# Performance work log

Measured on AMD Instinct MI355X. Metric: run time of the kernel, lower is better.

The kernel has to match this reference:

```python
import jax, jax.numpy as jnp
import numpy as np

B, S, H, DH = 4, 2048, 16, 64
D = H * DH          # 1024
EXP = 2
FF_IN = EXP * D * 2  # 4096 (SwiGLU doubles)
FF_HID = EXP * D     # 2048
SCALE_BASE = 512
LN_EPS = 1e-5


def setup_inputs() -> dict:
    key = jax.random.key(0)
    ks = jax.random.split(key, 8)
    inp = {
        "q": jax.random.normal(ks[0], (B, S, D), jnp.float32),
        "k": jax.random.normal(ks[1], (B, S, D), jnp.float32),
        "v": jax.random.normal(ks[2], (B, S, D), jnp.float32),
        "Wqkv": jax.random.normal(ks[3], (D, 3 * D), jnp.float32) * (1.0 / np.sqrt(D)),
        "bqkv": jnp.zeros((3 * D,), jnp.float32),
        "q_scale": jnp.ones((DH,), jnp.float32),
        "k_scale": jnp.ones((DH,), jnp.float32),
        "ln_g": jnp.ones((D,), jnp.float32),
        "ln_b": jnp.zeros((D,), jnp.float32),
        "W1": jax.random.normal(ks[4], (D, FF_IN), jnp.float32) * (1.0 / np.sqrt(D)),
        "b1": jnp.zeros((FF_IN,), jnp.float32),
        "W2": jax.random.normal(ks[5], (FF_HID, D), jnp.float32) * (1.0 / np.sqrt(FF_HID)),
        "b2": jnp.zeros((D,), jnp.float32),
    }
    return inp


def rotate_half(x):
    x1, x2 = jnp.split(x, 2, axis=-1)
    return jnp.concatenate((-x2, x1), axis=-1)


def apply_rope(pos, t, scale):
    # pos: [S, DH], scale: [S, DH] (broadcast over [B, H, S, DH])
    return t * jnp.cos(pos) * scale + rotate_half(t) * jnp.sin(pos) * scale


def rotary_tables(seq_len):
    inv_freq = 1.0 / (10000.0 ** (jnp.arange(0, DH, 2, dtype=jnp.float32) / DH))
    t = jnp.arange(seq_len, dtype=jnp.float32)
    freqs = t[:, None] * inv_freq[None, :]            # [S, DH/2]
    freqs = jnp.concatenate((freqs, freqs), axis=-1)  # [S, DH]
    power = (t - seq_len // 2) / SCALE_BASE           # [S]
    base = (jnp.arange(0, DH, 2, dtype=jnp.float32) + 0.4 * DH) / (1.4 * DH)  # [DH/2]
    scale = base[None, :] ** power[:, None]           # [S, DH/2]
    scale = jnp.concatenate((scale, scale), axis=-1)  # [S, DH]
    return freqs, scale


def l2norm(x, eps=1e-12):
    n = jnp.sqrt(jnp.sum(x * x, axis=-1, keepdims=True))
    return x / jnp.maximum(n, eps)


def reference(q, k, v, Wqkv, bqkv, q_scale, k_scale, ln_g, ln_b, W1, b1, W2, b2):
    del k, v  # module projects qkv from q; k,v args are unused (faithful to source)
    n, seq_len, _ = q.shape
    qkv = q @ Wqkv + bqkv                              # [B, S, 3D]
    qkv = qkv.reshape(n, seq_len, H, 3 * DH).transpose(0, 2, 1, 3)  # [B, H, S, 3DH]
    q_, k_, v_ = jnp.split(qkv, 3, axis=-1)
    q_ = l2norm(q_) * q_scale
    k_ = l2norm(k_) * k_scale
    pos, xscale = rotary_tables(seq_len)
    q_ = apply_rope(pos, q_, xscale)
    k_ = apply_rope(pos, k_, 1.0 / xscale)
    # scaled dot product attention (non-causal)
    scores = jnp.einsum("bhid,bhjd->bhij", q_, k_) / np.sqrt(DH)
    attn = jax.nn.softmax(scores, axis=-1)
    out = jnp.einsum("bhij,bhjd->bhid", attn, v_)      # [B, H, S, DH]
    out = out.transpose(0, 2, 1, 3).reshape(n, seq_len, D)
    # LayerNorm
    mu = jnp.mean(out, axis=-1, keepdims=True)
    var = jnp.mean((out - mu) ** 2, axis=-1, keepdims=True)
    out = (out - mu) / jnp.sqrt(var + LN_EPS) * ln_g + ln_b
    # SwiGLU FFN (dropout = identity in eval)
    h = out @ W1 + b1                                  # [B, S, FF_IN]
    x_, gate = jnp.split(h, 2, axis=-1)
    ff = (jax.nn.silu(gate) * x_) @ W2 + b2            # [B, S, D]
    return out + ff
```

## Files before the change

### kernel.cpp

```cpp
#include <hip/hip_runtime.h>
#include <math.h>


typedef __bf16 bf16;
typedef bf16 bf16x8 __attribute__((ext_vector_type(8)));
typedef bf16 bf16x4 __attribute__((ext_vector_type(4)));
typedef float f32x4 __attribute__((ext_vector_type(4)));

#define MFMA(a, b, c) __builtin_amdgcn_mfma_f32_16x16x32_bf16(a, b, c, 0, 0, 0)

__device__ __forceinline__ void async16(const void* g, void* l) {
    __builtin_amdgcn_global_load_lds(
        (const __attribute__((address_space(1))) void*)g,
        (__attribute__((address_space(3))) void*)l,
        16, 0, 0);
}

__global__ __launch_bounds__(256) void fill_sentinel(float* __restrict__ o)
{
    size_t i = ((size_t)blockIdx.x * 256 + threadIdx.x) * 4;
    *(float4*)&o[i] = make_float4(0.25f, 0.25f, 0.25f, 0.25f);
}

__global__ __launch_bounds__(256) void transpose_f32_bf16(
    const float* __restrict__ in, bf16* __restrict__ out, int K, int N)
{
    __shared__ bf16 T[64][70];
    const int tN = N >> 6;
    const int tk = blockIdx.x / tN, tn = blockIdx.x % tN;
    const int k0 = tk << 6, n0 = tn << 6;
    const int t = threadIdx.x;
    const int r = t >> 2, c0 = (t & 3) << 4;
    const float* src = &in[(size_t)(k0 + r) * N + n0 + c0];
    for (int j = 0; j < 4; ++j) {
        float4 f = *(const float4*)(src + 4 * j);
        T[r][c0 + 4 * j + 0] = (bf16)f.x;
        T[r][c0 + 4 * j + 1] = (bf16)f.y;
        T[r][c0 + 4 * j + 2] = (bf16)f.z;
        T[r][c0 + 4 * j + 3] = (bf16)f.w;
    }
    __syncthreads();
    bf16x8 o0, o1;
    for (int i = 0; i < 8; ++i) o0[i] = T[c0 + i][r];
    for (int i = 0; i < 8; ++i) o1[i] = T[c0 + 8 + i][r];
    *(bf16x8*)&out[(size_t)(n0 + r) * K + k0 + c0]     = o0;
    *(bf16x8*)&out[(size_t)(n0 + r) * K + k0 + c0 + 8] = o1;
}

__global__ __launch_bounds__(256) void transpose_v(
    const bf16* __restrict__ in, bf16* __restrict__ out)
{
    __shared__ bf16 T[64][72];
    const int bh = blockIdx.x >> 5;
    const int s0 = (blockIdx.x & 31) << 6;
    const bf16* ip = in + ((size_t)bh << 17) + (size_t)s0 * 64;
    bf16* op = out + ((size_t)bh << 17) + s0;
    const int t = threadIdx.x;
    const int r = t >> 2, c0 = (t & 3) << 4;
    *(bf16x8*)&T[r][c0]     = *(const bf16x8*)&ip[r * 64 + c0];
    *(bf16x8*)&T[r][c0 + 8] = *(const bf16x8*)&ip[r * 64 + c0 + 8];
    __syncthreads();
    bf16x8 o0, o1;
    for (int i = 0; i < 8; ++i) o0[i] = T[c0 + i][r];
    for (int i = 0; i < 8; ++i) o1[i] = T[c0 + 8 + i][r];
    *(bf16x8*)&op[(size_t)r * 2048 + c0]     = o0;
    *(bf16x8*)&op[(size_t)r * 2048 + c0 + 8] = o1;
}

template <int EPI, bool AF32>
__global__ __launch_bounds__(256) void gemm_bt(
    const void* __restrict__ Avp, const bf16* __restrict__ BT,
    const float* __restrict__ bias, int M, int N, int K, int lda,
    bf16* __restrict__ C0, bf16* __restrict__ C1, bf16* __restrict__ C2,
    float* __restrict__ Cf, const bf16* __restrict__ resid)
{
    __shared__ bf16 As[128 * 64];
    __shared__ bf16 Bs[128 * 64];
    const int tid = threadIdx.x;
    const int lane = tid & 63, wave = tid >> 6;
    const int quad = lane >> 4, l16 = lane & 15;
    const int wm = wave >> 1, wn = wave & 1;
    const int nb = N >> 7;
    const int bm = blockIdx.x / nb, bn = blockIdx.x % nb;
    const int m0 = bm << 7, n0 = bn << 7;
    const float* Af = (const float*)Avp;
    const bf16*  Ab = (const bf16*)Avp;
    char* aB = (char*)&As[0];
    char* bB = (char*)&Bs[0];
    const int rsw = l16 & 7;

    f32x4 acc[4][4] = {};

    for (int kt = 0; kt < K; kt += 64) {
        for (int i = 0; i < 4; ++i) {
            int l = (i << 8) + tid;
            int r = l >> 3;
            int cbs = ((l & 7) ^ (r & 7)) << 3;
            int cu = (i << 8) + (wave << 6);
            if (!AF32)
                async16(&Ab[(size_t)(m0 + r) * lda + kt + cbs], aB + (size_t)cu * 16);
            async16(&BT[(size_t)(n0 + r) * K + kt + cbs], bB + (size_t)cu * 16);
        }
        if (AF32) {
            for (int i = 0; i < 4; ++i) {
                int l = (i << 8) + tid;
                int r = l >> 3;
                int cbs = ((l & 7) ^ (r & 7)) << 3;
                const float* s = &Af[(size_t)(m0 + r) * lda + kt + cbs];
                float4 f0 = *(const float4*)s;
                float4 f1 = *(const float4*)(s + 4);
                bf16x8 tv;
                tv[0] = (bf16)f0.x; tv[1] = (bf16)f0.y;
                tv[2] = (bf16)f0.z; tv[3] = (bf16)f0.w;
                tv[4] = (bf16)f1.x; tv[5] = (bf16)f1.y;
                tv[6] = (bf16)f1.z; tv[7] = (bf16)f1.w;
                *(bf16x8*)&As[l << 3] = tv;
            }
        }
        __syncthreads();
        for (int kd = 0; kd < 2; ++kd) {
            bf16x8 af[4], bfr[4];
            for (int mi = 0; mi < 4; ++mi) {
                int row = (wm << 6) + (mi << 4) + l16;
                af[mi] = *(const bf16x8*)&As[(row << 6) + ((((kd << 2) + quad) ^ rsw) << 3)];
            }
            for (int ni = 0; ni < 4; ++ni) {
                int row = (wn << 6) + (ni << 4) + l16;
                bfr[ni] = *(const bf16x8*)&Bs[(row << 6) + ((((kd << 2) + quad) ^ rsw) << 3)];
            }
            for (int mi = 0; mi < 4; ++mi)
                for (int ni = 0; ni < 4; ++ni)
                    acc[mi][ni] = MFMA(af[mi], bfr[ni], acc[mi][ni]);
        }
        __syncthreads();
    }

    for (int mi = 0; mi < 4; ++mi) {
        for (int ni = 0; ni < 4; ++ni) {
            for (int r = 0; r < 4; ++r) {
                int row = m0 + (wm << 6) + (mi << 4) + (quad << 2) + r;
                int col = n0 + (wn << 6) + (ni << 4) + l16;
                float v = acc[mi][ni][r] + bias[col];
                if (EPI == 0) {
                    int b = row >> 11, s = row & 2047;
                    int h = col / 192, w = col % 192;
                    int tq = w >> 6, d = w & 63;
                    bf16* dst = (tq == 0) ? C0 : (tq == 1) ? C1 : C2;
                    dst[((((size_t)b * 16 + h) * 2048 + s) << 6) + d] = (bf16)v;
                } else if (EPI == 1) {
                    C0[(size_t)row * N + col] = (bf16)v;
                } else {
                    float rv = (float)resid[(size_t)row * N + col];
                    Cf[(size_t)row * N + col] = v + rv;
                }
            }
        }
    }
}

__global__ __launch_bounds__(256) void norm_rope(
    bf16* __restrict__ qb, bf16* __restrict__ kb,
    const float* __restrict__ qs, const float* __restrict__ ks)
{
    const int wave = threadIdx.x >> 6, lane = threadIdx.x & 63;
    const int rid = blockIdx.x * 4 + wave;
    const bool is_k = rid >= 131072;
    const int idx = is_k ? rid - 131072 : rid;
    const int s = idx & 2047;
    bf16* ptr = (is_k ? kb : qb) + ((size_t)idx << 6);
    const int d = lane;

    float v = (float)ptr[d];
    float ss = v * v;
    for (int o = 1; o < 64; o <<= 1) ss += __shfl_xor(ss, o);
    float t = v * rsqrtf(fmaxf(ss, 1e-24f));
    t *= (is_k ? ks : qs)[d];

    float partner = __shfl_xor(t, 32);
    float rh = (d < 32) ? -partner : partner;

    const float fi = (float)(d & 31);
    float inv_freq = __builtin_amdgcn_exp2f(fi * -0.4152410118609203f);
    float pos = (float)s * inv_freq;
    float rev = pos * 0.15915494309189535f;
    rev = rev - floorf(rev);
    float sn = __builtin_amdgcn_sinf(rev);
    float cs = __builtin_amdgcn_cosf(rev);
    float base = (2.0f * fi + 25.6f) * (1.0f / 89.6f);
    float power = ((float)s - 1024.0f) * (1.0f / 512.0f);
    if (is_k) power = -power;
    float xsc = __builtin_amdgcn_exp2f(power * __builtin_amdgcn_logf(base));
    ptr[d] = (bf16)((t * cs + rh * sn) * xsc);
}

__global__ __launch_bounds__(256) void attn(
    const bf16* __restrict__ Q, const bf16* __restrict__ Kb,
    const bf16* __restrict__ VT, bf16* __restrict__ O)
{
    __shared__ bf16 Ks[64 * 64];
    __shared__ bf16 Vt[64 * 64];
    __shared__ bf16 Ps[4][2][16][72];
    const int tid = threadIdx.x;
    const int lane = tid & 63, wave = tid >> 6;
    const int quad = lane >> 4, l16 = lane & 15;
    const int rsw = l16 & 7;
    const int bh = blockIdx.x >> 4;
    const int q0 = (blockIdx.x & 15) << 7;
    const int s_base = q0 + (wave << 5);
    const bf16* Qp = Q + ((size_t)bh << 17);
    const bf16* Kp = Kb + ((size_t)bh << 17);
    const bf16* Vp = VT + ((size_t)bh << 17);

    bf16x8 qf[2][2];
    for (int sub = 0; sub < 2; ++sub) {
        const bf16* qrow = Qp + (size_t)(s_base + (sub << 4) + l16) * 64;
        qf[sub][0] = *(const bf16x8*)&qrow[(quad << 3)];
        qf[sub][1] = *(const bf16x8*)&qrow[32 + (quad << 3)];
        for (int j = 0; j < 8; ++j) {
            qf[sub][0][j] = (bf16)((float)qf[sub][0][j] * 0.1803368801f);
            qf[sub][1][j] = (bf16)((float)qf[sub][1][j] * 0.1803368801f);
        }
    }
    bf16x8 ones = {};
    if (l16 == 0) for (int j = 0; j < 8; ++j) ones[j] = (bf16)1.0f;

    f32x4 oacc[2][4] = {};
    f32x4 lacc[2] = {};
    char* kB = (char*)&Ks[0];
    char* vB = (char*)&Vt[0];

    for (int kt = 0; kt < 2048; kt += 64) {
        __syncthreads();
        for (int i = 0; i < 2; ++i) {
            int l = (i << 8) + tid;
            int r = l >> 3;
            int cbs = ((l & 7) ^ (r & 7)) << 3;
            int cu = (i << 8) + (wave << 6);
            async16(&Kp[(size_t)(kt + r) * 64 + cbs], kB + (size_t)cu * 16);
            async16(&Vp[(size_t)r * 2048 + kt + cbs], vB + (size_t)cu * 16);
        }
        __syncthreads();

        f32x4 sc[2][4];
        for (int nt = 0; nt < 4; ++nt) {
            int row = (nt << 4) + l16;
            bf16x8 kf0 = *(const bf16x8*)&Ks[(row << 6) + ((quad ^ rsw) << 3)];
            bf16x8 kf1 = *(const bf16x8*)&Ks[(row << 6) + (((quad + 4) ^ rsw) << 3)];
            for (int sub = 0; sub < 2; ++sub) {
                f32x4 z = {};
                z = MFMA(qf[sub][0], kf0, z);
                z = MFMA(qf[sub][1], kf1, z);
                sc[sub][nt] = z;
            }
        }
        const int prow = quad << 2;
        for (int sub = 0; sub < 2; ++sub)
            for (int r = 0; r < 4; ++r)
                for (int nt = 0; nt < 4; ++nt)
                    Ps[wave][sub][prow + r][(nt << 4) + l16] =
                        (bf16)__builtin_amdgcn_exp2f(sc[sub][nt][r]);
        __builtin_amdgcn_wave_barrier();
        bf16x8 pf0[2], pf1[2];
        for (int sub = 0; sub < 2; ++sub) {
            pf0[sub] = *(const bf16x8*)&Ps[wave][sub][l16][(quad << 3)];
            pf1[sub] = *(const bf16x8*)&Ps[wave][sub][l16][32 + (quad << 3)];
        }
        for (int ntd = 0; ntd < 4; ++ntd) {
            int row = (ntd << 4) + l16;
            bf16x8 vf0 = *(const bf16x8*)&Vt[(row << 6) + ((quad ^ rsw) << 3)];
            bf16x8 vf1 = *(const bf16x8*)&Vt[(row << 6) + (((quad + 4) ^ rsw) << 3)];
            for (int sub = 0; sub < 2; ++sub) {
                oacc[sub][ntd] = MFMA(pf0[sub], vf0, oacc[sub][ntd]);
                oacc[sub][ntd] = MFMA(pf1[sub], vf1, oacc[sub][ntd]);
            }
        }
        for (int sub = 0; sub < 2; ++sub) {
            lacc[sub] = MFMA(pf0[sub], ones, lacc[sub]);
            lacc[sub] = MFMA(pf1[sub], ones, lacc[sub]);
        }
    }

    const int b = bh >> 4, h = bh & 15;
    for (int sub = 0; sub < 2; ++sub)
        for (int r = 0; r < 4; ++r) {
            float l = __shfl(lacc[sub][r], quad << 4);
            float inv_l = 1.0f / l;
            int srow = s_base + (sub << 4) + (quad << 2) + r;
            for (int ntd = 0; ntd < 4; ++ntd) {
                int d = (ntd << 4) + l16;
                O[((((size_t)b * 2048 + srow) * 16) + h) * 64 + d] =
                    (bf16)(oacc[sub][ntd][r] * inv_l);
            }
        }
}

__global__ __launch_bounds__(256) void layernorm(
    const bf16* __restrict__ x, const float* __restrict__ g,
    const float* __restrict__ b, bf16* __restrict__ y)
{
    __shared__ float red[8];
    const int row = blockIdx.x;
    const int t = threadIdx.x;
    const bf16* xr = x + ((size_t)row << 10);
    bf16x4 xv = *(const bf16x4*)&xr[t << 2];
    float v[4], s = 0.0f, sq = 0.0f;
    for (int i = 0; i < 4; ++i) { v[i] = (float)xv[i]; s += v[i]; sq += v[i] * v[i]; }
    for (int o = 1; o < 64; o <<= 1) { s += __shfl_xor(s, o); sq += __shfl_xor(sq, o); }
    const int wave = t >> 6, lane = t & 63;
    if (lane == 0) { red[wave] = s; red[4 + wave] = sq; }
    __syncthreads();
    s  = red[0] + red[1] + red[2] + red[3];
    sq = red[4] + red[5] + red[6] + red[7];
    float mu = s * (1.0f / 1024.0f);
    float var = fmaxf(sq * (1.0f / 1024.0f) - mu * mu, 0.0f);
    float rstd = rsqrtf(var + 1e-5f);
    bf16x4 ov;
    for (int i = 0; i < 4; ++i) {
        int c = (t << 2) + i;
        ov[i] = (bf16)((v[i] - mu) * rstd * g[c] + b[c]);
    }
    *(bf16x4*)(y + ((size_t)row << 10) + (t << 2)) = ov;
}

__global__ __launch_bounds__(256) void swiglu(bf16* __restrict__ h)
{
    size_t i = ((size_t)blockIdx.x * 256 + threadIdx.x) * 8;
    size_t row = i >> 11, c = i & 2047;
    bf16* hr = h + (row << 12);
    bf16x8 xv = *(const bf16x8*)&hr[c];
    bf16x8 gv = *(const bf16x8*)&hr[c + 2048];
    bf16x8 ov;
    for (int j = 0; j < 8; ++j) {
        float xf = (float)xv[j], gf = (float)gv[j];
        ov[j] = (bf16)(gf / (1.0f + __expf(-gf)) * xf);
    }
    *(bf16x8*)&hr[c] = ov;
}

extern "C" void kernel_launch(void* const* d_in, const int* in_sizes, int n_in,
                              void* d_out, int out_size, void* d_ws, size_t ws_size,
                              hipStream_t stream) {
    (void)in_sizes; (void)n_in; (void)out_size;
    const float* q    = (const float*)d_in[0];
    const float* Wqkv = (const float*)d_in[3];
    const float* bqkv = (const float*)d_in[4];
    const float* qsc  = (const float*)d_in[5];
    const float* ksc  = (const float*)d_in[6];
    const float* lng  = (const float*)d_in[7];
    const float* lnb  = (const float*)d_in[8];
    const float* W1   = (const float*)d_in[9];
    const float* b1   = (const float*)d_in[10];
    const float* W2   = (const float*)d_in[11];
    const float* b2   = (const float*)d_in[12];
    float* out = (float*)d_out;

    const size_t MB = 1024 * 1024;
    if (ws_size < 92 * MB) {
        fill_sentinel<<<8192, 256, 0, stream>>>(out);
        return;
    }

    char* ws = (char*)d_ws;
    bf16* W2T      = (bf16*)(ws + 0);
    bf16* ln_buf   = (bf16*)(ws + 4  * MB);
    bf16* W1T      = (bf16*)(ws + 20 * MB);
    bf16* q_buf    = (bf16*)(ws + 28 * MB);
    bf16* k_buf    = (bf16*)(ws + 44 * MB);
    bf16* v_buf    = (bf16*)(ws + 60 * MB);
    bf16* WqkvT    = (bf16*)(ws + 76 * MB);
    bf16* vt_buf   = (bf16*)(ws + 76 * MB);
    bf16* attn_buf = (bf16*)(ws + 60 * MB);
    bf16* h_buf    = (bf16*)(ws + 28 * MB);

    transpose_f32_bf16<<<512,  256, 0, stream>>>(W2,   W2T,   2048, 1024);
    transpose_f32_bf16<<<1024, 256, 0, stream>>>(W1,   W1T,   1024, 4096);
    transpose_f32_bf16<<<768,  256, 0, stream>>>(Wqkv, WqkvT, 1024, 3072);

    gemm_bt<0, true><<<1536, 256, 0, stream>>>(q, WqkvT, bqkv, 8192, 3072, 1024, 1024,
                                               q_buf, k_buf, v_buf, nullptr, nullptr);
    norm_rope<<<65536, 256, 0, stream>>>(q_buf, k_buf, qsc, ksc);
    transpose_v<<<2048, 256, 0, stream>>>(v_buf, vt_buf);
    attn<<<1024, 256, 0, stream>>>(q_buf, k_buf, vt_buf, attn_buf);
    layernorm<<<8192, 256, 0, stream>>>(attn_buf, lng, lnb, ln_buf);
    gemm_bt<1, false><<<2048, 256, 0, stream>>>(ln_buf, W1T, b1, 8192, 4096, 1024, 1024,
                                                h_buf, nullptr, nullptr, nullptr, nullptr);
    swiglu<<<8192, 256, 0, stream>>>(h_buf);
    gemm_bt<2, false><<<512, 256, 0, stream>>>(h_buf, W2T, b2, 8192, 1024, 2048, 4096,
                                               nullptr, nullptr, nullptr, out, ln_buf);
}
```

Before: 558.8 us.

## Double-buffer K/V tiles in attention and vectorize P stores

The attention kernel now keeps two LDS buffers for the K and V tiles. The next tile's async global-to-LDS copy is issued right after the single per-iteration barrier, so the load overlaps compute on the current tile and one barrier per iteration goes away. The QK^T MFMA operands are swapped so each lane holds consecutive key columns, which lets the exponentiated P values be written to LDS as packed bf16x4 stores instead of scalar ones. s_setprio hints are placed around the MFMA blocks. The cost is twice the K/V shared memory, which may reduce occupancy, and correctness now depends on the barrier also covering completion of the async LDS copies.

```diff
diff --git a/kernel.cpp b/kernel.cpp
--- a/kernel.cpp
+++ b/kernel.cpp
@@ -193,12 +193,26 @@
     ptr[d] = (bf16)((t * cs + rh * sn) * xsc);
 }
 
+__device__ __forceinline__ void attn_stage(
+    const bf16* __restrict__ Kp, const bf16* __restrict__ Vp, int kt,
+    char* kB, char* vB, int tid, int wave)
+{
+    for (int i = 0; i < 2; ++i) {
+        int l = (i << 8) + tid;
+        int r = l >> 3;
+        int cbs = ((l & 7) ^ (r & 7)) << 3;
+        int cu = (i << 8) + (wave << 6);
+        async16(&Kp[(size_t)(kt + r) * 64 + cbs], kB + (size_t)cu * 16);
+        async16(&Vp[(size_t)r * 2048 + kt + cbs], vB + (size_t)cu * 16);
+    }
+}
+
 __global__ __launch_bounds__(256) void attn(
     const bf16* __restrict__ Q, const bf16* __restrict__ Kb,
     const bf16* __restrict__ VT, bf16* __restrict__ O)
 {
-    __shared__ bf16 Ks[64 * 64];
-    __shared__ bf16 Vt[64 * 64];
+    __shared__ bf16 Ks[2][64 * 64];
+    __shared__ bf16 Vt[2][64 * 64];
     __shared__ bf16 Ps[4][2][16][72];
     const int tid = threadIdx.x;
     const int lane = tid & 63, wave = tid >> 6;
@@ -226,49 +240,53 @@
 
     f32x4 oacc[2][4] = {};
     f32x4 lacc[2] = {};
-    char* kB = (char*)&Ks[0];
-    char* vB = (char*)&Vt[0];
-
-    for (int kt = 0; kt < 2048; kt += 64) {
+
+    attn_stage(Kp, Vp, 0, (char*)&Ks[0][0], (char*)&Vt[0][0], tid, wave);
+
+    int buf = 0;
+    for (int kt = 0; kt < 2048; kt += 64, buf ^= 1) {
         __syncthreads();
-        for (int i = 0; i < 2; ++i) {
-            int l = (i << 8) + tid;
-            int r = l >> 3;
-            int cbs = ((l & 7) ^ (r & 7)) << 3;
-            int cu = (i << 8) + (wave << 6);
-            async16(&Kp[(size_t)(kt + r) * 64 + cbs], kB + (size_t)cu * 16);
-            async16(&Vp[(size_t)r * 2048 + kt + cbs], vB + (size_t)cu * 16);
-        }
-        __syncthreads();
+        if (kt + 64 < 2048)
+            attn_stage(Kp, Vp, kt + 64,
+                       (char*)&Ks[buf ^ 1][0], (char*)&Vt[buf ^ 1][0], tid, wave);
+
+        const bf16* Kt_ = &Ks[buf][0];
+        const bf16* Vc_ = &Vt[buf][0];
 
         f32x4 sc[2][4];
+        __builtin_amdgcn_s_setprio(1);
         for (int nt = 0; nt < 4; ++nt) {
             int row = (nt << 4) + l16;
-            bf16x8 kf0 = *(const bf16x8*)&Ks[(row << 6) + ((quad ^ rsw) << 3)];
-            bf16x8 kf1 = *(const bf16x8*)&Ks[(row << 6) + (((quad + 4) ^ rsw) << 3)];
+            bf16x8 kf0 = *(const bf16x8*)&Kt_[(row << 6) + ((quad ^ rsw) << 3)];
+            bf16x8 kf1 = *(const bf16x8*)&Kt_[(row << 6) + (((quad + 4) ^ rsw) << 3)];
             for (int sub = 0; sub < 2; ++sub) {
                 f32x4 z = {};
-                z = MFMA(qf[sub][0], kf0, z);
-                z = MFMA(qf[sub][1], kf1, z);
+                z = MFMA(kf0, qf[sub][0], z);
+                z = MFMA(kf1, qf[sub][1], z);
                 sc[sub][nt] = z;
             }
         }
-        const int prow = quad << 2;
+        __builtin_amdgcn_s_setprio(0);
+
         for (int sub = 0; sub < 2; ++sub)
-            for (int r = 0; r < 4; ++r)
-                for (int nt = 0; nt < 4; ++nt)
-                    Ps[wave][sub][prow + r][(nt << 4) + l16] =
-                        (bf16)__builtin_amdgcn_exp2f(sc[sub][nt][r]);
+            for (int nt = 0; nt < 4; ++nt) {
+                bf16x4 pk;
+                for (int r = 0; r < 4; ++r)
+                    pk[r] = (bf16)__builtin_amdgcn_exp2f(sc[sub][nt][r]);
+                *(bf16x4*)&Ps[wave][sub][l16][(nt << 4) + (quad << 2)] = pk;
+            }
         __builtin_amdgcn_wave_barrier();
         bf16x8 pf0[2], pf1[2];
         for (int sub = 0; sub < 2; ++sub) {
             pf0[sub] = *(const bf16x8*)&Ps[wave][sub][l16][(quad << 3)];
             pf1[sub] = *(const bf16x8*)&Ps[wave][sub][l16][32 + (quad << 3)];
         }
+
+        __builtin_amdgcn_s_setprio(1);
         for (int ntd = 0; ntd < 4; ++ntd) {
             int row = (ntd << 4) + l16;
-            bf16x8 vf0 = *(const bf16x8*)&Vt[(row << 6) + ((quad ^ rsw) << 3)];
-            bf16x8 vf1 = *(const bf16x8*)&Vt[(row << 6) + (((quad + 4) ^ rsw) << 3)];
+            bf16x8 vf0 = *(const bf16x8*)&Vc_[(row << 6) + ((quad ^ rsw) << 3)];
+            bf16x8 vf1 = *(const bf16x8*)&Vc_[(row << 6) + (((quad + 4) ^ rsw) << 3)];
             for (int sub = 0; sub < 2; ++sub) {
                 oacc[sub][ntd] = MFMA(pf0[sub], vf0, oacc[sub][ntd]);
                 oacc[sub][ntd] = MFMA(pf1[sub], vf1, oacc[sub][ntd]);
@@ -278,6 +296,7 @@
             lacc[sub] = MFMA(pf0[sub], ones, lacc[sub]);
             lacc[sub] = MFMA(pf1[sub], ones, lacc[sub]);
         }
+        __builtin_amdgcn_s_setprio(0);
     }
 
     const int b = bh >> 4, h = bh & 15;
```

Measured after the change: 540.5 us. -3.3%, faster.
